# Kernel tuning notes

Measured on AMD Instinct MI355X. Metric: run time of the kernel, lower is better.

The kernel has to match this reference:

```python
import jax, jax.numpy as jnp
import numpy as np

N_BATCH = 4096
D_FEAT = 64
N_CLASSES = 10
DET_EPS = 1e-8


def setup_inputs() -> dict:
    key = jax.random.key(0)
    k1, k2, k3 = jax.random.split(key, 3)
    # small-magnitude means and variances bounded away from 0 keep the
    # KL values (and hence sigmoid(KL)) in a numerically meaningful range
    mu = jax.random.normal(k1, (N_BATCH, D_FEAT), dtype=jnp.float32) * 0.1
    var = jax.random.uniform(k2, (N_BATCH, D_FEAT), dtype=jnp.float32) + 0.5
    labels = jax.random.randint(k3, (N_BATCH,), 0, N_CLASSES)
    return {"mu": mu, "var": var, "labels": labels}


def _pairwise_kl(mu, var):
    """K[i, j] = KL(N(mu_i, diag(var_i)) || N(mu_j, diag(var_j))),
    matching the original's kl_mvn on the row/col tiling, but computed
    elementwise/matmul instead of dense diag_embed + inv/det (same math:
    inv(diag(S1)) @ diag(S0) summed == sum(S0/S1); det(diag(S)) == prod(S))."""
    D = mu.shape[1]
    inv_var = 1.0 / var                                   # [N, D]
    # tr term: sum_d var_i,d / var_j,d
    tr = var @ inv_var.T                                  # [N, N]
    # det term: det(S1)/ (det(S0)+eps) with diagonal determinants = products
    p = jnp.prod(var, axis=1)                             # [N]
    det = p[None, :] / (p[:, None] + DET_EPS)             # [N, N]
    # quad term: sum_d (mu_j - mu_i)^2 / var_j,d, expanded into matmuls
    mu_sq = mu * mu                                       # [N, D]
    quad = (mu_sq @ inv_var.T
            - 2.0 * (mu @ (mu * inv_var).T)
            + jnp.sum(mu_sq * inv_var, axis=1)[None, :])  # [N, N]
    return 0.5 * (tr + det + quad - D)


def reference(mu, var, labels):
    N = mu.shape[0]
    K = _pairwise_kl(mu, var)                 # KL(i -> j)
    sym = 0.5 * (K + K.T)                     # symmetric_kl over the pair grid
    logits = jax.nn.sigmoid(sym)              # [N, N]

    same = labels[:, None] == labels[None, :]
    off_diag = ~jnp.eye(N, dtype=bool)        # logits_mask: zero out diagonal
    p_mask = (same & off_diag).astype(logits.dtype)
    n_mask = ((~same) & off_diag).astype(logits.dtype)

    pos = logits * p_mask
    neg = logits * n_mask
    return (jnp.mean(pos), jnp.mean(neg), jnp.sum(pos), jnp.sum(neg))
```

## Files before the change

kernel.cpp:

```cpp
#include <hip/hip_runtime.h>


#define N 4096
#define D 64
#define KH 256
#define TILES 64
#define NBLK 2080
#define DET_EPS 1e-8f

typedef short bf16x8 __attribute__((ext_vector_type(8)));
typedef float f32x16 __attribute__((ext_vector_type(16)));

#define WS_H    0
#define WS_HP   (N * KH * 2)
#define WS_PSL  (2 * N * KH * 2)
#define WS_PART (WS_PSL + N * 16)

static __device__ __forceinline__ unsigned short f2bf(float x) {
  unsigned int u = __float_as_uint(x);
  unsigned int r = (u + 0x7FFFu + ((u >> 16) & 1u)) >> 16;
  return (unsigned short)r;
}

__global__ __launch_bounds__(256) void precompute_kernel(
    const float* __restrict__ mu, const float* __restrict__ var,
    const int* __restrict__ labels,
    unsigned short* __restrict__ Hf, unsigned short* __restrict__ Hpf,
    float4* __restrict__ PSL) {
  const int t = threadIdx.x;
  const int lane = t & 63;
  const int w = t >> 6;
  const int r = blockIdx.x * 4 + w;

  const float m = mu[r * D + lane];
  const float v = var[r * D + lane];
  const float g0 = 1.0f / v;
  const float f0 = v + m * m;
  const float f1 = -2.0f * m;
  const float g1 = m * g0;

  const size_t base = (size_t)(r >> 5) * 8192 + (size_t)(lane >> 2) * 512
                      + (size_t)(r & 31) * 16 + (size_t)(lane & 3) * 4;
  const ushort4 hf = make_ushort4(f2bf(f0), f2bf(f1), f2bf(g0), f2bf(g1));
  const ushort4 hg = make_ushort4(hf.z, hf.w, hf.x, hf.y);
  *(ushort4*)&Hf[base] = hf;
  *(ushort4*)&Hpf[base] = hg;

  float p = v;
  float s = m * m * g0;
  #pragma unroll
  for (int off = 1; off < 64; off <<= 1) {
    p *= __shfl_xor(p, off);
    s += __shfl_xor(s, off);
  }
  if (lane == 0) {
    PSL[r] = make_float4(p, 1.0f / (p + DET_EPS), s, (float)labels[r]);
  }
}

__global__ __launch_bounds__(256, 4) void pair_kernel(
    const unsigned short* __restrict__ Hf, const unsigned short* __restrict__ Hpf,
    const float4* __restrict__ PSL, float* __restrict__ partial) {
  __shared__ float4 sPi[64];
  __shared__ float4 sPj[64];
  __shared__ float red[8];

  int L = (int)blockIdx.x;
  int it = (int)(64.5f - sqrtf(64.5f * 64.5f - 2.0f * (float)L));
  while (it > 0 && L < it * 64 - it * (it - 1) / 2) --it;
  while (L >= (it + 1) * 64 - (it + 1) * it / 2) ++it;
  const int jt = it + (L - (it * 64 - it * (it - 1) / 2));
  const int i0 = it * 64, j0 = jt * 64;

  const int t = threadIdx.x;
  const int lane = t & 63;
  const int w = t >> 6;
  const int sr = w >> 1, sc = w & 1;

  if (t < 64) sPi[t] = PSL[i0 + t];
  else if (t < 128) sPj[t - 64] = PSL[j0 + t - 64];

  const int slot = (lane & 31) * 16 + (lane >> 5) * 8;
  const unsigned short* pa = Hf + (size_t)(i0 / 32 + sr) * 8192 + slot;
  const unsigned short* pb = Hpf + (size_t)(j0 / 32 + sc) * 8192 + slot;

  f32x16 C = {};
  #pragma unroll
  for (int k = 0; k < 16; ++k) {
    const bf16x8 a = *(const bf16x8*)(pa + k * 512);
    const bf16x8 b = *(const bf16x8*)(pb + k * 512);
    C = __builtin_amdgcn_mfma_f32_32x32x16_bf16(a, b, C, 0, 0, 0);
  }

  __syncthreads();

  const int l31 = lane & 31;
  const int jloc = sc * 32 + l31;
  const int j = j0 + jloc;
  const float4 pj = sPj[jloc];
  const int rbase = 4 * (lane >> 5);
  float pos = 0.0f, neg = 0.0f;
  #pragma unroll
  for (int r = 0; r < 16; ++r) {
    const int row = (r & 3) + 8 * (r >> 2) + rbase;
    const int iloc = sr * 32 + row;
    const int i = i0 + iloc;
    if (i < j) {
      const float4 pi = sPi[iloc];
      const float sym = 0.25f * (C[r] + pi.z + pj.z
                                 + pj.x * pi.y + pi.x * pj.y - 128.0f);
      const float sig = __builtin_amdgcn_rcpf(1.0f + __expf(-sym));
      if (pi.w == pj.w) pos += sig; else neg += sig;
    }
  }

  #pragma unroll
  for (int off = 32; off > 0; off >>= 1) {
    pos += __shfl_down(pos, off);
    neg += __shfl_down(neg, off);
  }
  if (lane == 0) { red[w] = pos; red[4 + w] = neg; }
  __syncthreads();
  if (t == 0) {
    partial[L]        = red[0] + red[1] + red[2] + red[3];
    partial[NBLK + L] = red[4] + red[5] + red[6] + red[7];
  }
}

__global__ __launch_bounds__(256) void finalize_kernel(
    const float* __restrict__ partial, float* __restrict__ out) {
  __shared__ float redp[4], redn[4];
  const int t = threadIdx.x;
  const int lane = t & 63, w = t >> 6;
  float p = 0.0f, n = 0.0f;
  for (int i = t; i < NBLK; i += 256) {
    p += partial[i];
    n += partial[NBLK + i];
  }
  #pragma unroll
  for (int off = 32; off > 0; off >>= 1) {
    p += __shfl_down(p, off);
    n += __shfl_down(n, off);
  }
  if (lane == 0) { redp[w] = p; redn[w] = n; }
  __syncthreads();
  if (t == 0) {
    const float pos = 2.0f * (redp[0] + redp[1] + redp[2] + redp[3]);
    const float neg = 2.0f * (redn[0] + redn[1] + redn[2] + redn[3]);
    out[0] = pos * (1.0f / 16777216.0f);
    out[1] = neg * (1.0f / 16777216.0f);
    out[2] = pos;
    out[3] = neg;
  }
}

extern "C" void kernel_launch(void* const* d_in, const int* in_sizes, int n_in,
                              void* d_out, int out_size, void* d_ws, size_t ws_size,
                              hipStream_t stream) {
  const float* mu = (const float*)d_in[0];
  const float* var = (const float*)d_in[1];
  const int* labels = (const int*)d_in[2];
  float* out = (float*)d_out;
  char* ws = (char*)d_ws;

  unsigned short* Hf = (unsigned short*)(ws + WS_H);
  unsigned short* Hpf = (unsigned short*)(ws + WS_HP);
  float4* PSL = (float4*)(ws + WS_PSL);
  float* partial = (float*)(ws + WS_PART);

  precompute_kernel<<<dim3(N / 4), dim3(256), 0, stream>>>(mu, var, labels, Hf, Hpf, PSL);
  pair_kernel<<<dim3(NBLK), dim3(256), 0, stream>>>(Hf, Hpf, PSL, partial);
  finalize_kernel<<<dim3(1), dim3(256), 0, stream>>>(partial, out);
}
```

Measured before the change: 80.84 us.

## Enlarge pair tiles to 128x128 with 2x2 MFMA per wave and drop Hpf buffer

```diff
diff --git a/kernel.cpp b/kernel.cpp
--- a/kernel.cpp
+++ b/kernel.cpp
@@ -4,16 +4,16 @@
 #define N 4096
 #define D 64
 #define KH 256
-#define TILES 64
-#define NBLK 2080
+#define MT 128
+#define TILES2 32
+#define NBLK2 528
 #define DET_EPS 1e-8f
 
 typedef short bf16x8 __attribute__((ext_vector_type(8)));
 typedef float f32x16 __attribute__((ext_vector_type(16)));
 
 #define WS_H    0
-#define WS_HP   (N * KH * 2)
-#define WS_PSL  (2 * N * KH * 2)
+#define WS_PSL  (N * KH * 2)
 #define WS_PART (WS_PSL + N * 16)
 
 static __device__ __forceinline__ unsigned short f2bf(float x) {
@@ -22,11 +22,14 @@
   return (unsigned short)r;
 }
 
+static __device__ __forceinline__ f32x16 mfma_bf16(bf16x8 a, bf16x8 b, f32x16 c) {
+  return __builtin_amdgcn_mfma_f32_32x32x16_bf16(a, b, c, 0, 0, 0);
+}
+
 __global__ __launch_bounds__(256) void precompute_kernel(
     const float* __restrict__ mu, const float* __restrict__ var,
     const int* __restrict__ labels,
-    unsigned short* __restrict__ Hf, unsigned short* __restrict__ Hpf,
-    float4* __restrict__ PSL) {
+    unsigned short* __restrict__ Hf, float4* __restrict__ PSL) {
   const int t = threadIdx.x;
   const int lane = t & 63;
   const int w = t >> 6;
@@ -41,10 +44,7 @@
 
   const size_t base = (size_t)(r >> 5) * 8192 + (size_t)(lane >> 2) * 512
                       + (size_t)(r & 31) * 16 + (size_t)(lane & 3) * 4;
-  const ushort4 hf = make_ushort4(f2bf(f0), f2bf(f1), f2bf(g0), f2bf(g1));
-  const ushort4 hg = make_ushort4(hf.z, hf.w, hf.x, hf.y);
-  *(ushort4*)&Hf[base] = hf;
-  *(ushort4*)&Hpf[base] = hg;
+  *(ushort4*)&Hf[base] = make_ushort4(f2bf(f0), f2bf(f1), f2bf(g0), f2bf(g1));
 
   float p = v;
   float s = m * m * g0;
@@ -54,63 +54,80 @@
     s += __shfl_xor(s, off);
   }
   if (lane == 0) {
-    PSL[r] = make_float4(p, 1.0f / (p + DET_EPS), s, (float)labels[r]);
+    PSL[r] = make_float4(p, 1.0f / (p + DET_EPS), 0.25f * s - 16.0f,
+                         (float)labels[r]);
   }
 }
 
-__global__ __launch_bounds__(256, 4) void pair_kernel(
-    const unsigned short* __restrict__ Hf, const unsigned short* __restrict__ Hpf,
+__global__ __launch_bounds__(256, 2) void pair_kernel(
+    const unsigned short* __restrict__ Hf,
     const float4* __restrict__ PSL, float* __restrict__ partial) {
-  __shared__ float4 sPi[64];
-  __shared__ float4 sPj[64];
+  __shared__ float4 sPi[128];
+  __shared__ float4 sPj[128];
   __shared__ float red[8];
 
   int L = (int)blockIdx.x;
-  int it = (int)(64.5f - sqrtf(64.5f * 64.5f - 2.0f * (float)L));
-  while (it > 0 && L < it * 64 - it * (it - 1) / 2) --it;
-  while (L >= (it + 1) * 64 - (it + 1) * it / 2) ++it;
-  const int jt = it + (L - (it * 64 - it * (it - 1) / 2));
-  const int i0 = it * 64, j0 = jt * 64;
+  int it = (int)(32.5f - sqrtf(32.5f * 32.5f - 2.0f * (float)L));
+  while (it > 0 && L < it * TILES2 - it * (it - 1) / 2) --it;
+  while (L >= (it + 1) * TILES2 - (it + 1) * it / 2) ++it;
+  const int jt = it + (L - (it * TILES2 - it * (it - 1) / 2));
+  const int i0 = it * MT, j0 = jt * MT;
 
   const int t = threadIdx.x;
   const int lane = t & 63;
   const int w = t >> 6;
   const int sr = w >> 1, sc = w & 1;
 
-  if (t < 64) sPi[t] = PSL[i0 + t];
-  else if (t < 128) sPj[t - 64] = PSL[j0 + t - 64];
-
-  const int slot = (lane & 31) * 16 + (lane >> 5) * 8;
-  const unsigned short* pa = Hf + (size_t)(i0 / 32 + sr) * 8192 + slot;
-  const unsigned short* pb = Hpf + (size_t)(j0 / 32 + sc) * 8192 + slot;
-
-  f32x16 C = {};
-  #pragma unroll
-  for (int k = 0; k < 16; ++k) {
-    const bf16x8 a = *(const bf16x8*)(pa + k * 512);
-    const bf16x8 b = *(const bf16x8*)(pb + k * 512);
-    C = __builtin_amdgcn_mfma_f32_32x32x16_bf16(a, b, C, 0, 0, 0);
-  }
-
+  if (t < 128) sPi[t] = PSL[i0 + t];
+  else sPj[t - 128] = PSL[j0 + t - 128];
   __syncthreads();
 
   const int l31 = lane & 31;
-  const int jloc = sc * 32 + l31;
-  const int j = j0 + jloc;
-  const float4 pj = sPj[jloc];
-  const int rbase = 4 * (lane >> 5);
+  const int slot = l31 * 16 + (lane >> 5) * 8;
+  const unsigned short* pa = Hf + (size_t)(i0 / 32 + sr * 2) * 8192 + slot;
+  const unsigned short* pb = Hf + (size_t)(j0 / 32 + sc * 2) * 8192 + slot;
+
+  const bool active = !(it == jt && w == 2);
+
+  f32x16 C00 = {}, C01 = {}, C10 = {}, C11 = {};
   float pos = 0.0f, neg = 0.0f;
-  #pragma unroll
-  for (int r = 0; r < 16; ++r) {
-    const int row = (r & 3) + 8 * (r >> 2) + rbase;
-    const int iloc = sr * 32 + row;
-    const int i = i0 + iloc;
-    if (i < j) {
-      const float4 pi = sPi[iloc];
-      const float sym = 0.25f * (C[r] + pi.z + pj.z
-                                 + pj.x * pi.y + pi.x * pj.y - 128.0f);
-      const float sig = __builtin_amdgcn_rcpf(1.0f + __expf(-sym));
-      if (pi.w == pj.w) pos += sig; else neg += sig;
+
+  if (active) {
+    #pragma unroll 4
+    for (int k = 0; k < 16; ++k) {
+      const bf16x8 a0 = *(const bf16x8*)(pa + k * 512);
+      const bf16x8 a1 = *(const bf16x8*)(pa + 8192 + k * 512);
+      const bf16x8 c0 = *(const bf16x8*)(pb + k * 512);
+      const bf16x8 c1 = *(const bf16x8*)(pb + 8192 + k * 512);
+      const bf16x8 b0 = __builtin_shufflevector(c0, c0, 2, 3, 0, 1, 6, 7, 4, 5);
+      const bf16x8 b1 = __builtin_shufflevector(c1, c1, 2, 3, 0, 1, 6, 7, 4, 5);
+      C00 = mfma_bf16(a0, b0, C00);
+      C01 = mfma_bf16(a0, b1, C01);
+      C10 = mfma_bf16(a1, b0, C10);
+      C11 = mfma_bf16(a1, b1, C11);
+    }
+
+    const int rbase = 4 * (lane >> 5);
+    #pragma unroll
+    for (int mn = 0; mn < 4; ++mn) {
+      const int m = mn >> 1, n = mn & 1;
+      const f32x16 C = (mn == 0) ? C00 : (mn == 1) ? C01 : (mn == 2) ? C10 : C11;
+      const int jloc = (sc * 2 + n) * 32 + l31;
+      const int j = j0 + jloc;
+      const float4 pj = sPj[jloc];
+      #pragma unroll
+      for (int r = 0; r < 16; ++r) {
+        const int row = (r & 3) + 8 * (r >> 2) + rbase;
+        const int iloc = (sr * 2 + m) * 32 + row;
+        const int i = i0 + iloc;
+        if (i < j) {
+          const float4 pi = sPi[iloc];
+          const float det = pj.x * pi.y + pi.x * pj.y;
+          const float sym = 0.25f * (C[r] + det) + pi.z + pj.z;
+          const float sig = __builtin_amdgcn_rcpf(1.0f + __expf(-sym));
+          if (pi.w == pj.w) pos += sig; else neg += sig;
+        }
+      }
     }
   }
 
@@ -122,8 +139,8 @@
   if (lane == 0) { red[w] = pos; red[4 + w] = neg; }
   __syncthreads();
   if (t == 0) {
-    partial[L]        = red[0] + red[1] + red[2] + red[3];
-    partial[NBLK + L] = red[4] + red[5] + red[6] + red[7];
+    partial[L]         = red[0] + red[1] + red[2] + red[3];
+    partial[NBLK2 + L] = red[4] + red[5] + red[6] + red[7];
   }
 }
 
@@ -133,9 +150,9 @@
   const int t = threadIdx.x;
   const int lane = t & 63, w = t >> 6;
   float p = 0.0f, n = 0.0f;
-  for (int i = t; i < NBLK; i += 256) {
+  for (int i = t; i < NBLK2; i += 256) {
     p += partial[i];
-    n += partial[NBLK + i];
+    n += partial[NBLK2 + i];
   }
   #pragma unroll
   for (int off = 32; off > 0; off >>= 1) {
@@ -164,11 +181,10 @@
   char* ws = (char*)d_ws;
 
   unsigned short* Hf = (unsigned short*)(ws + WS_H);
-  unsigned short* Hpf = (unsigned short*)(ws + WS_HP);
   float4* PSL = (float4*)(ws + WS_PSL);
   float* partial = (float*)(ws + WS_PART);
 
-  precompute_kernel<<<dim3(N / 4), dim3(256), 0, stream>>>(mu, var, labels, Hf, Hpf, PSL);
-  pair_kernel<<<dim3(NBLK), dim3(256), 0, stream>>>(Hf, Hpf, PSL, partial);
+  precompute_kernel<<<dim3(N / 4), dim3(256), 0, stream>>>(mu, var, labels, Hf, PSL);
+  pair_kernel<<<dim3(NBLK2), dim3(256), 0, stream>>>(Hf, PSL, partial);
   finalize_kernel<<<dim3(1), dim3(256), 0, stream>>>(partial, out);
 }
```

After: 78.83 us (median of 2 runs). -2.5%, faster.
